# Kernel tuning notes

Measured on AMD Instinct MI355X. Metric: run time of the kernel, lower is better.

## Reference

```python
import jax, jax.numpy as jnp
import numpy as np

N_NODES = 100000
N_EDGES = 800000
IN_DIM = 128
HID = 128
EMB = 2 * HID  # 256, embedding_dim = hidden_dim * 2
N_CLS = 16


def _glorot(key, shape):
    fan_in, fan_out = shape
    lim = jnp.sqrt(6.0 / (fan_in + fan_out)).astype(jnp.float32)
    return jax.random.uniform(key, shape, jnp.float32, -lim, lim)


def setup_inputs() -> dict:
    key = jax.random.key(0)
    ks = jax.random.split(key, 12)
    x = jax.random.normal(ks[0], (N_NODES, IN_DIM), jnp.float32)
    edge_index = jax.random.randint(ks[1], (2, N_EDGES), 0, N_NODES, jnp.int64)
    return {
        "x": x,
        "edge_index": edge_index,
        # layer 1: GraphConv(IN_DIM -> HID)
        "W_rel1": _glorot(ks[2], (IN_DIM, HID)),
        "W_root1": _glorot(ks[3], (IN_DIM, HID)),
        "b1": jnp.zeros((HID,), jnp.float32),
        # layer 2: GraphConv(HID -> EMB)
        "W_rel2": _glorot(ks[4], (HID, EMB)),
        "W_root2": _glorot(ks[5], (HID, EMB)),
        "b2": jnp.zeros((EMB,), jnp.float32),
        # layer 3: GraphConv(EMB -> N_CLS)
        "W_rel3": _glorot(ks[6], (EMB, N_CLS)),
        "W_root3": _glorot(ks[7], (EMB, N_CLS)),
        "b3": jnp.zeros((N_CLS,), jnp.float32),
    }


def _graph_conv(x, src, dst, W_rel, W_root, b):
    # PyG GraphConv: out = lin_rel(sum_{j in N(i)} x_j) + lin_root(x_i)
    agg = jax.ops.segment_sum(x[src], dst, num_segments=N_NODES)  # [N, F_in]
    return agg @ W_rel + x @ W_root + b


def reference(x, edge_index, W_rel1, W_root1, b1, W_rel2, W_root2, b2,
              W_rel3, W_root3, b3):
    src, dst = edge_index[0], edge_index[1]
    h = jax.nn.relu(_graph_conv(x, src, dst, W_rel1, W_root1, b1))
    # dropout skipped: eval mode (training=False)
    h = jax.nn.relu(_graph_conv(h, src, dst, W_rel2, W_root2, b2))
    h = _graph_conv(h, src, dst, W_rel3, W_root3, b3)
    return jax.nn.log_softmax(h, axis=1)
```

## Files before the change

### kernel.cpp

```cpp
#include <hip/hip_runtime.h>

#define NN 100000
#define NE 800000
#define NPAD 100096
#define OCT 12544

typedef __attribute__((ext_vector_type(8))) __bf16 bf16x8;
typedef __attribute__((ext_vector_type(4))) float f32x4;

__device__ __forceinline__ uint f2bf(float f) {
  uint u = __float_as_uint(f);
  return (u + 0x7fffu + ((u >> 16) & 1u)) >> 16;
}
__device__ __forceinline__ float bflo(uint u) { return __uint_as_float(u << 16); }
__device__ __forceinline__ float bfhi(uint u) { return __uint_as_float(u & 0xffff0000u); }

__device__ __forceinline__ bf16x8 cvt8(float4 a, float4 b) {
  uint4 u;
  u.x = f2bf(a.x) | (f2bf(a.y) << 16);
  u.y = f2bf(a.z) | (f2bf(a.w) << 16);
  u.z = f2bf(b.x) | (f2bf(b.y) << 16);
  u.w = f2bf(b.z) | (f2bf(b.w) << 16);
  return *(bf16x8*)&u;
}


__device__ __forceinline__ bf16x8 ldfrag(const ushort* base, int row, int kb) {
  int off = (row << 8) + (kb ^ ((row & 15) << 4));
  return *(const bf16x8*)((const char*)base + off);
}

__global__ __launch_bounds__(512, 4) void k_fuse1(
    const float* __restrict__ x, ushort* __restrict__ Y1, ushort* __restrict__ Z1,
    const float* __restrict__ Wr1, const float* __restrict__ Wo1,
    const float* __restrict__ Wr2, const float* __restrict__ Wo2,
    const float* __restrict__ Wr3, const float* __restrict__ Wo3,
    ushort* __restrict__ wt, const int* __restrict__ dst, int* __restrict__ deg) {
  __shared__ ushort sW[128 * 128];
  int b = blockIdx.x;
  int tid = threadIdx.x;

  if (b >= 2352) {
    int idx = 32768 + (b - 2352) * 512 + tid;
    float v;
    if (idx < 98304) {
      const float* W;
      int base;
      if (idx < 65536) { W = Wr2; base = 32768; }
      else { W = Wo2; base = 65536; }
      int li = idx - base;
      int o = li >> 7, k = li & 127;
      k = (k & 7) * 16 + (k >> 3);
      v = W[(size_t)k * 256 + o];
    } else {
      int li = idx - 98304;
      int o = li >> 8, p = li & 255;
      int k = (p & 15) * 16 + (p >> 4);
      v = (o < 16) ? Wr3[(size_t)k * 16 + o] : Wo3[(size_t)k * 16 + (o - 16)];
    }
    wt[idx] = (ushort)f2bf(v);
    return;
  }
  if (b >= 784) {
    int hb = b - 784;
    int xcd = hb & 7, chunk = hb >> 3;
    int e0 = chunk * 4096 + tid;
#pragma unroll
    for (int i = 0; i < 8; ++i) {
      int e = e0 + i * 512;
      if (e < NE) {
        int d = dst[e];
        if (d / OCT == xcd) atomicAdd(&deg[d], 1);
      }
    }
    return;
  }

  int half = (b >> 3) & 1;
  int pr = (b >> 4) * 8 + (b & 7);
  if (pr >= NPAD / 256) return;
  int r0 = pr * 256;

  int lane = tid & 63, wid = tid >> 6;
  int cl = lane & 15, hi = lane >> 4;
  int arow0 = r0 + wid * 32 + cl;
  int arow1 = arow0 + 16;
  const float* px0 = x + (size_t)(arow0 < NN ? arow0 : NN - 1) * 128;
  const float* px1 = x + (size_t)(arow1 < NN ? arow1 : NN - 1) * 128;

  float4 F0[2][2], F1[2][2];
#pragma unroll
  for (int s = 0; s < 2; ++s) {
    F0[s][0] = *(const float4*)(px0 + s * 32 + hi * 8);
    F0[s][1] = *(const float4*)(px0 + s * 32 + hi * 8 + 4);
    F1[s][0] = *(const float4*)(px1 + s * 32 + hi * 8);
    F1[s][1] = *(const float4*)(px1 + s * 32 + hi * 8 + 4);
  }

  {
    const float* Wsrc = half ? Wo1 : Wr1;
    int o = tid & 127;
    int kp = tid >> 7;
#pragma unroll
    for (int it = 0; it < 16; ++it) {
      int k0 = (it * 4 + kp) * 2;
      float w0 = Wsrc[(size_t)k0 * 128 + o];
      float w1 = Wsrc[(size_t)(k0 + 1) * 128 + o];
      uint u = f2bf(w0) | (f2bf(w1) << 16);
      int byte = (o << 8) + ((((k0 >> 3) << 4) ^ ((o & 15) << 4))) + (k0 & 7) * 2;
      *(uint*)((char*)sW + byte) = u;
    }
  }
  __syncthreads();

  f32x4 zero = {0.f, 0.f, 0.f, 0.f};
  f32x4 acc0[8], acc1[8];
#pragma unroll
  for (int j = 0; j < 8; ++j) { acc0[j] = zero; acc1[j] = zero; }

#pragma unroll
  for (int ks = 0; ks < 4; ++ks) {
    const int p2 = ks & 1;
    bf16x8 A0 = cvt8(F0[p2][0], F0[p2][1]);
    bf16x8 A1 = cvt8(F1[p2][0], F1[p2][1]);
    int kb = ks * 64 + hi * 16;
#pragma unroll
    for (int j = 0; j < 8; ++j) {
      bf16x8 wf = ldfrag(sW, j * 16 + cl, kb);
      acc0[j] = __builtin_amdgcn_mfma_f32_16x16x32_bf16(A0, wf, acc0[j], 0, 0, 0);
      acc1[j] = __builtin_amdgcn_mfma_f32_16x16x32_bf16(A1, wf, acc1[j], 0, 0, 0);
    }
    if (ks < 2) {
      F0[p2][0] = *(const float4*)(px0 + (ks + 2) * 32 + hi * 8);
      F0[p2][1] = *(const float4*)(px0 + (ks + 2) * 32 + hi * 8 + 4);
      F1[p2][0] = *(const float4*)(px1 + (ks + 2) * 32 + hi * 8);
      F1[p2][1] = *(const float4*)(px1 + (ks + 2) * 32 + hi * 8 + 4);
    }
  }

  ushort* tgt = half ? Z1 : Y1;
#pragma unroll
  for (int i = 0; i < 2; ++i) {
#pragma unroll
    for (int reg = 0; reg < 4; ++reg) {
      int row = r0 + wid * 32 + i * 16 + hi * 4 + reg;
      if (row < NN) {
        float a[8];
#pragma unroll
        for (int j = 0; j < 8; ++j) a[j] = i ? acc1[j][reg] : acc0[j][reg];
        uint4 u;
        u.x = f2bf(a[0]) | (f2bf(a[1]) << 16);
        u.y = f2bf(a[2]) | (f2bf(a[3]) << 16);
        u.z = f2bf(a[4]) | (f2bf(a[5]) << 16);
        u.w = f2bf(a[6]) | (f2bf(a[7]) << 16);
        *(uint4*)(tgt + (size_t)row * 128 + cl * 8) = u;
      }
    }
  }
}

__global__ void k_scan_partial(const int* __restrict__ deg, int* __restrict__ bsum, int N) {
  __shared__ int s[256];
  int b = blockIdx.x, t = threadIdx.x;
  int base = b * 1024 + t * 4;
  int v = 0;
#pragma unroll
  for (int i = 0; i < 4; ++i) { int idx = base + i; if (idx < N) v += deg[idx]; }
  s[t] = v; __syncthreads();
  for (int o = 128; o > 0; o >>= 1) { if (t < o) s[t] += s[t + o]; __syncthreads(); }
  if (t == 0) bsum[b] = s[0];
}

__global__ void k_scan_final(const int* __restrict__ deg, const int* __restrict__ bsum,
                             int* __restrict__ offsets, int* __restrict__ cursor,
                             int N, int NB) {
  __shared__ int s2[128];
  __shared__ int s[256];
  int b = blockIdx.x, t = threadIdx.x;
  if (t < 128) s2[t] = (t < NB) ? bsum[t] : 0;
  __syncthreads();
  for (int o = 1; o < 128; o <<= 1) {
    int add = (t < 128 && t >= o) ? s2[t - o] : 0;
    __syncthreads();
    if (t < 128) s2[t] += add;
    __syncthreads();
  }
  int bpre = (b > 0) ? s2[b - 1] : 0;
  if (b == 0 && t == 0) offsets[N] = s2[NB - 1];

  int base = b * 1024 + t * 4;
  int v[4];
#pragma unroll
  for (int i = 0; i < 4; ++i) { int idx = base + i; v[i] = (idx < N) ? deg[idx] : 0; }
  int tsum = v[0] + v[1] + v[2] + v[3];
  s[t] = tsum; __syncthreads();
  for (int o = 1; o < 256; o <<= 1) {
    int add = (t >= o) ? s[t - o] : 0;
    __syncthreads();
    s[t] += add;
    __syncthreads();
  }
  int run = s[t] - tsum + bpre;
#pragma unroll
  for (int i = 0; i < 4; ++i) {
    int idx = base + i;
    if (idx < N) { offsets[idx] = run; cursor[idx] = run; }
    run += v[i];
  }
}

__global__ __launch_bounds__(256) void k_scatter(const int* __restrict__ src,
                                                 const int* __restrict__ dst,
                                                 int* __restrict__ cursor,
                                                 int* __restrict__ csr_src) {
  int xcd = blockIdx.x & 7, chunk = blockIdx.x >> 3;
  int e0 = chunk * 2048 + threadIdx.x;
#pragma unroll
  for (int i = 0; i < 8; ++i) {
    int e = e0 + i * 256;
    if (e < NE) {
      int d = dst[e];
      if (d / OCT == xcd) {
        int pos = atomicAdd(&cursor[d], 1);
        csr_src[pos] = src[e];
      }
    }
  }
}

#define ACC8(q)                      \
  do {                               \
    acc[0] += bflo(q.x); acc[1] += bfhi(q.x); \
    acc[2] += bflo(q.y); acc[3] += bfhi(q.y); \
    acc[4] += bflo(q.z); acc[5] += bfhi(q.z); \
    acc[6] += bflo(q.w); acc[7] += bfhi(q.w); \
  } while (0)

#define GATHER8(X4)                                               \
  int j = o0;                                                     \
  if (j + 7 < o1) {                                               \
    uint4 q0 = X4[(size_t)csr[j] * 16 + fl];                      \
    uint4 q1 = X4[(size_t)csr[j + 1] * 16 + fl];                  \
    uint4 q2 = X4[(size_t)csr[j + 2] * 16 + fl];                  \
    uint4 q3 = X4[(size_t)csr[j + 3] * 16 + fl];                  \
    uint4 q4 = X4[(size_t)csr[j + 4] * 16 + fl];                  \
    uint4 q5 = X4[(size_t)csr[j + 5] * 16 + fl];                  \
    uint4 q6 = X4[(size_t)csr[j + 6] * 16 + fl];                  \
    uint4 q7 = X4[(size_t)csr[j + 7] * 16 + fl];                  \
    j += 8;                                                       \
    while (j + 7 < o1) {                                          \
      uint4 p0 = X4[(size_t)csr[j] * 16 + fl];                    \
      uint4 p1 = X4[(size_t)csr[j + 1] * 16 + fl];                \
      uint4 p2 = X4[(size_t)csr[j + 2] * 16 + fl];                \
      uint4 p3 = X4[(size_t)csr[j + 3] * 16 + fl];                \
      uint4 p4 = X4[(size_t)csr[j + 4] * 16 + fl];                \
      uint4 p5 = X4[(size_t)csr[j + 5] * 16 + fl];                \
      uint4 p6 = X4[(size_t)csr[j + 6] * 16 + fl];                \
      uint4 p7 = X4[(size_t)csr[j + 7] * 16 + fl];                \
      j += 8;                                                     \
      ACC8(q0); ACC8(q1); ACC8(q2); ACC8(q3);                     \
      ACC8(q4); ACC8(q5); ACC8(q6); ACC8(q7);                     \
      q0 = p0; q1 = p1; q2 = p2; q3 = p3;                         \
      q4 = p4; q5 = p5; q6 = p6; q7 = p7;                         \
    }                                                             \
    ACC8(q0); ACC8(q1); ACC8(q2); ACC8(q3);                       \
    ACC8(q4); ACC8(q5); ACC8(q6); ACC8(q7);                       \
  }                                                               \
  if (j + 3 < o1) {                                               \
    uint4 q0 = X4[(size_t)csr[j] * 16 + fl];                      \
    uint4 q1 = X4[(size_t)csr[j + 1] * 16 + fl];                  \
    uint4 q2 = X4[(size_t)csr[j + 2] * 16 + fl];                  \
    uint4 q3 = X4[(size_t)csr[j + 3] * 16 + fl];                  \
    j += 4;                                                       \
    ACC8(q0); ACC8(q1); ACC8(q2); ACC8(q3);                       \
  }                                                               \
  for (; j < o1; ++j) {                                           \
    uint4 q = X4[(size_t)csr[j] * 16 + fl];                       \
    ACC8(q);                                                      \
  }

__global__ __launch_bounds__(256) void k_agg_relu(const ushort* __restrict__ Y1,
                                                  const ushort* __restrict__ Z1,
                                                  const int* __restrict__ offsets,
                                                  const int* __restrict__ csr,
                                                  const float* __restrict__ bias,
                                                  ushort* __restrict__ h1) {
  int tid = threadIdx.x;
  int sg = tid >> 4, fl = tid & 15;
  int n = blockIdx.x * 16 + sg;
  if (n >= NN) return;
  int o0 = offsets[n], o1 = offsets[n + 1];
  const uint4* X4 = (const uint4*)Y1;
  float acc[8];
#pragma unroll
  for (int k = 0; k < 8; ++k) acc[k] = 0.f;
  GATHER8(X4)
  uint4 zown = ((const uint4*)Z1)[(size_t)n * 16 + fl];
  float z[8] = {bflo(zown.x), bfhi(zown.x), bflo(zown.y), bfhi(zown.y),
                bflo(zown.z), bfhi(zown.z), bflo(zown.w), bfhi(zown.w)};
  float r[8];
#pragma unroll
  for (int jj = 0; jj < 8; ++jj) {
    r[jj] = fmaxf(acc[jj] + z[jj] + bias[jj * 16 + fl], 0.f);
  }
  uint4 o;
  o.x = f2bf(r[0]) | (f2bf(r[1]) << 16);
  o.y = f2bf(r[2]) | (f2bf(r[3]) << 16);
  o.z = f2bf(r[4]) | (f2bf(r[5]) << 16);
  o.w = f2bf(r[6]) | (f2bf(r[7]) << 16);
  ((uint4*)h1)[(size_t)n * 16 + fl] = o;
}

__global__ __launch_bounds__(256) void k_aggbf(const ushort* __restrict__ X,
                                               const int* __restrict__ offsets,
                                               const int* __restrict__ csr,
                                               ushort* __restrict__ out) {
  int tid = threadIdx.x;
  int sg = tid >> 4, fl = tid & 15;
  int n = blockIdx.x * 16 + sg;
  if (n >= NN) return;
  int o0 = offsets[n], o1 = offsets[n + 1];
  const uint4* X4 = (const uint4*)X;
  float acc[8];
#pragma unroll
  for (int k = 0; k < 8; ++k) acc[k] = 0.f;
  GATHER8(X4)
  uint4 o;
  o.x = f2bf(acc[0]) | (f2bf(acc[1]) << 16);
  o.y = f2bf(acc[2]) | (f2bf(acc[3]) << 16);
  o.z = f2bf(acc[4]) | (f2bf(acc[5]) << 16);
  o.w = f2bf(acc[6]) | (f2bf(acc[7]) << 16);
  ((uint4*)out)[(size_t)n * 16 + fl] = o;
}

__global__ __launch_bounds__(512, 4) void k_gemm2l3(
    const ushort* __restrict__ Aagg, const ushort* __restrict__ Aroot,
    const ushort* __restrict__ Wrelt, const ushort* __restrict__ Wroott,
    const float* __restrict__ bias2, const ushort* __restrict__ Wt3,
    const float* __restrict__ bias3, ushort* __restrict__ y3b, float* __restrict__ z) {
  __shared__ ushort sW[256 * 128];
  int tid = threadIdx.x;
  int r0 = blockIdx.x * 128;
  int lane = tid & 63, wid = tid >> 6;
  int cl = lane & 15, hi = lane >> 4;
  int arow = r0 + wid * 16 + cl;
  const ushort* pa = Aagg + (size_t)arow * 128 + hi * 8;
  const ushort* pr = Aroot + (size_t)arow * 128 + hi * 8;

  bf16x8 Aa[2], Ar[2];
  Aa[0] = *(const bf16x8*)(pa);
  Aa[1] = *(const bf16x8*)(pa + 32);
  Ar[0] = *(const bf16x8*)(pr);
  Ar[1] = *(const bf16x8*)(pr + 32);

  {
    const char* gw = (const char*)Wrelt;
#pragma unroll
    for (int i = 0; i < 8; ++i) {
      int L = (tid + i * 512) << 4;
      int row = L >> 8;
      int gb = L ^ ((row & 15) << 4);
      __builtin_amdgcn_global_load_lds((const __attribute__((address_space(1))) void*)(gw + gb),
                                       (__attribute__((address_space(3))) void*)((char*)sW + L), 16, 0, 0);
    }
  }
  __syncthreads();

  f32x4 zero = {0.f, 0.f, 0.f, 0.f};
  f32x4 acc[16];
#pragma unroll
  for (int j = 0; j < 16; ++j) acc[j] = zero;

#pragma unroll
  for (int ks = 0; ks < 4; ++ks) {
    const int p = ks & 1;
    int kb = ks * 64 + hi * 16;
#pragma unroll
    for (int j = 0; j < 16; ++j) {
      bf16x8 wf = ldfrag(sW, j * 16 + cl, kb);
      acc[j] = __builtin_amdgcn_mfma_f32_16x16x32_bf16(Aa[p], wf, acc[j], 0, 0, 0);
    }
    if (ks < 2) Aa[p] = *(const bf16x8*)(pa + (ks + 2) * 32);
  }
  __syncthreads();

  {
    const char* gw = (const char*)Wroott;
#pragma unroll
    for (int i = 0; i < 8; ++i) {
      int L = (tid + i * 512) << 4;
      int row = L >> 8;
      int gb = L ^ ((row & 15) << 4);
      __builtin_amdgcn_global_load_lds((const __attribute__((address_space(1))) void*)(gw + gb),
                                       (__attribute__((address_space(3))) void*)((char*)sW + L), 16, 0, 0);
    }
  }
  __syncthreads();

#pragma unroll
  for (int ks = 0; ks < 4; ++ks) {
    const int p = ks & 1;
    int kb = ks * 64 + hi * 16;
#pragma unroll
    for (int j = 0; j < 16; ++j) {
      bf16x8 wf = ldfrag(sW, j * 16 + cl, kb);
      acc[j] = __builtin_amdgcn_mfma_f32_16x16x32_bf16(Ar[p], wf, acc[j], 0, 0, 0);
    }
    if (ks < 2) Ar[p] = *(const bf16x8*)(pr + (ks + 2) * 32);
  }
  __syncthreads();

  {
    float bv[16];
#pragma unroll
    for (int j = 0; j < 16; ++j) bv[j] = bias2[j * 16 + cl];
#pragma unroll
    for (int reg = 0; reg < 4; ++reg) {
      int rr = hi * 4 + reg;
      float v[16];
#pragma unroll
      for (int j = 0; j < 16; ++j) v[j] = fmaxf(acc[j][reg] + bv[j], 0.f);
      uint4 a, bq;
      a.x = f2bf(v[0]) | (f2bf(v[1]) << 16);
      a.y = f2bf(v[2]) | (f2bf(v[3]) << 16);
      a.z = f2bf(v[4]) | (f2bf(v[5]) << 16);
      a.w = f2bf(v[6]) | (f2bf(v[7]) << 16);
      bq.x = f2bf(v[8]) | (f2bf(v[9]) << 16);
      bq.y = f2bf(v[10]) | (f2bf(v[11]) << 16);
      bq.z = f2bf(v[12]) | (f2bf(v[13]) << 16);
      bq.w = f2bf(v[14]) | (f2bf(v[15]) << 16);
      int rowb = (wid * 16 + rr) * 512;
      *(uint4*)((char*)sW + rowb + ((cl * 32 + 0) ^ (rr << 4))) = a;
      *(uint4*)((char*)sW + rowb + ((cl * 32 + 16) ^ (rr << 4))) = bq;
    }
  }
  __syncthreads();

  f32x4 ay = zero, az = zero;
  const ushort* w3a = Wt3 + cl * 256 + hi * 8;
  const ushort* w3b = Wt3 + (16 + cl) * 256 + hi * 8;
#pragma unroll
  for (int ks = 0; ks < 8; ++ks) {
    int c = ks * 4 + hi;
    bf16x8 a = *(const bf16x8*)((const char*)sW + (wid * 16 + cl) * 512 + ((c * 16) ^ (cl << 4)));
    bf16x8 b0 = *(const bf16x8*)(w3a + ks * 32);
    bf16x8 b1 = *(const bf16x8*)(w3b + ks * 32);
    ay = __builtin_amdgcn_mfma_f32_16x16x32_bf16(a, b0, ay, 0, 0, 0);
    az = __builtin_amdgcn_mfma_f32_16x16x32_bf16(a, b1, az, 0, 0, 0);
  }
  float bv3 = bias3[cl];
#pragma unroll
  for (int reg = 0; reg < 4; ++reg) {
    int row = r0 + wid * 16 + hi * 4 + reg;
    if (row < NN) {
      y3b[(size_t)row * 16 + cl] = (ushort)f2bf(ay[reg]);
      z[(size_t)row * 16 + cl] = az[reg] + bv3;
    }
  }
}

__global__ void k_agg16lsm(const int* __restrict__ offsets, const int* __restrict__ csr,
                           const ushort* __restrict__ y3b, float* __restrict__ out) {
  int t = blockIdx.x * 256 + threadIdx.x;
  if (t >= NN * 8) return;
  int n = t >> 3, g = t & 7;
  int o0 = offsets[n], o1 = offsets[n + 1];
  float a0 = 0.f, a1 = 0.f;
  const uint* Y = (const uint*)y3b;
  int j = o0;
  if (j + 3 < o1) {
    uint u0 = Y[(size_t)csr[j] * 8 + g];
    uint u1 = Y[(size_t)csr[j + 1] * 8 + g];
    uint u2 = Y[(size_t)csr[j + 2] * 8 + g];
    uint u3 = Y[(size_t)csr[j + 3] * 8 + g];
    j += 4;
    while (j + 3 < o1) {
      uint v0 = Y[(size_t)csr[j] * 8 + g];
      uint v1 = Y[(size_t)csr[j + 1] * 8 + g];
      uint v2 = Y[(size_t)csr[j + 2] * 8 + g];
      uint v3 = Y[(size_t)csr[j + 3] * 8 + g];
      j += 4;
      a0 += bflo(u0) + bflo(u1) + bflo(u2) + bflo(u3);
      a1 += bfhi(u0) + bfhi(u1) + bfhi(u2) + bfhi(u3);
      u0 = v0; u1 = v1; u2 = v2; u3 = v3;
    }
    a0 += bflo(u0) + bflo(u1) + bflo(u2) + bflo(u3);
    a1 += bfhi(u0) + bfhi(u1) + bfhi(u2) + bfhi(u3);
  }
  for (; j < o1; ++j) {
    uint u = Y[(size_t)csr[j] * 8 + g];
    a0 += bflo(u); a1 += bfhi(u);
  }
  float v0 = out[n * 16 + g * 2] + a0;
  float v1 = out[n * 16 + g * 2 + 1] + a1;
  float m = fmaxf(v0, v1);
#pragma unroll
  for (int mask = 1; mask < 8; mask <<= 1) m = fmaxf(m, __shfl_xor(m, mask));
  float s = __expf(v0 - m) + __expf(v1 - m);
#pragma unroll
  for (int mask = 1; mask < 8; mask <<= 1) s += __shfl_xor(s, mask);
  float ls = __logf(s);
  out[n * 16 + g * 2] = v0 - m - ls;
  out[n * 16 + g * 2 + 1] = v1 - m - ls;
}

extern "C" void kernel_launch(void* const* d_in, const int* in_sizes, int n_in,
                              void* d_out, int out_size, void* d_ws, size_t ws_size,
                              hipStream_t stream) {
  const float* x = (const float*)d_in[0];
  const int* ei = (const int*)d_in[1];
  const float* Wrel1 = (const float*)d_in[2];
  const float* Wroot1 = (const float*)d_in[3];
  const float* b1 = (const float*)d_in[4];
  const float* Wrel2 = (const float*)d_in[5];
  const float* Wroot2 = (const float*)d_in[6];
  const float* b2 = (const float*)d_in[7];
  const float* Wrel3 = (const float*)d_in[8];
  const float* Wroot3 = (const float*)d_in[9];
  const float* b3 = (const float*)d_in[10];
  float* out = (float*)d_out;

  char* ws = (char*)d_ws;
  size_t off = 0;
  auto alloc = [&](size_t bytes) {
    void* p = ws + off;
    off += (bytes + 255) / 256 * 256;
    return p;
  };
  int* deg = (int*)alloc((size_t)NN * 4);
  int* offsets = (int*)alloc((size_t)(NN + 1) * 4);
  int* cursor = (int*)alloc((size_t)NN * 4);
  int* bsum = (int*)alloc(128 * 4);
  int* csr = (int*)alloc((size_t)NE * 4);
  ushort* Y1 = (ushort*)alloc((size_t)NN * 128 * 2);
  ushort* Z1 = (ushort*)alloc((size_t)NN * 128 * 2);
  ushort* aggb = (ushort*)alloc((size_t)NPAD * 128 * 2);
  ushort* h1b = (ushort*)alloc((size_t)NPAD * 128 * 2);
  ushort* y3b = (ushort*)alloc((size_t)NN * 16 * 2);
  ushort* wt = (ushort*)alloc((size_t)106496 * 2);
  ushort *Wr2t = wt + 32768, *Wo2t = wt + 65536;
  ushort* Wt3 = wt + 98304;

  const int* src = ei;
  const int* dst = ei + NE;

  hipMemsetAsync(deg, 0, (size_t)NN * 4, stream);
  k_fuse1<<<2496, 512, 0, stream>>>(x, Y1, Z1, Wrel1, Wroot1, Wrel2, Wroot2, Wrel3,
                                    Wroot3, wt, dst, deg);

  int NB = (NN + 1023) / 1024;
  k_scan_partial<<<NB, 256, 0, stream>>>(deg, bsum, NN);
  k_scan_final<<<NB, 256, 0, stream>>>(deg, bsum, offsets, cursor, NN, NB);
  int nchunk = (NE + 2047) / 2048;
  k_scatter<<<8 * nchunk, 256, 0, stream>>>(src, dst, cursor, csr);

  k_agg_relu<<<NN / 16, 256, 0, stream>>>(Y1, Z1, offsets, csr, b1, h1b);
  k_aggbf<<<(NN + 15) / 16, 256, 0, stream>>>(h1b, offsets, csr, aggb);
  k_gemm2l3<<<NPAD / 128, 512, 0, stream>>>(aggb, h1b, Wr2t, Wo2t, b2, Wt3, b3, y3b, out);
  k_agg16lsm<<<(NN * 8 + 255) / 256, 256, 0, stream>>>(offsets, csr, y3b, out);
}
```

Before: 224.0 us.

## Sort nodes into degree bins so aggregation warps process similar-degree nodes

Builds a degree histogram during the scan, prefix-sums it, and scatters node ids into a degree-binned permutation. The three aggregation kernels then visit nodes in that permuted order, so nodes sharing a wavefront have similar neighbor counts. This is meant to reduce divergence and load imbalance inside wavefronts. It adds two small kernels plus atomics, gives up locality of node-ordered output writes and Z1 reads, and the binning atomics make the order nondeterministic.

```diff
diff --git a/kernel.cpp b/kernel.cpp
--- a/kernel.cpp
+++ b/kernel.cpp
@@ -159,9 +159,11 @@
   }
 }
 
-__global__ void k_scan_partial(const int* __restrict__ deg, int* __restrict__ bsum, int N) {
+__global__ void k_scan_partial(const int* __restrict__ deg, int* __restrict__ bsum,
+                               int* __restrict__ dbins, int N) {
   __shared__ int s[256];
   int b = blockIdx.x, t = threadIdx.x;
+  if (b == 0 && t < 64) dbins[t] = 0;
   int base = b * 1024 + t * 4;
   int v = 0;
 #pragma unroll
@@ -173,11 +175,13 @@
 
 __global__ void k_scan_final(const int* __restrict__ deg, const int* __restrict__ bsum,
                              int* __restrict__ offsets, int* __restrict__ cursor,
-                             int N, int NB) {
+                             int* __restrict__ dbins, int N, int NB) {
   __shared__ int s2[128];
   __shared__ int s[256];
+  __shared__ int hist[64];
   int b = blockIdx.x, t = threadIdx.x;
   if (t < 128) s2[t] = (t < NB) ? bsum[t] : 0;
+  if (t < 64) hist[t] = 0;
   __syncthreads();
   for (int o = 1; o < 128; o <<= 1) {
     int add = (t < 128 && t >= o) ? s2[t - o] : 0;
@@ -191,7 +195,11 @@
   int base = b * 1024 + t * 4;
   int v[4];
 #pragma unroll
-  for (int i = 0; i < 4; ++i) { int idx = base + i; v[i] = (idx < N) ? deg[idx] : 0; }
+  for (int i = 0; i < 4; ++i) {
+    int idx = base + i;
+    v[i] = (idx < N) ? deg[idx] : 0;
+    if (idx < N) atomicAdd(&hist[v[i] < 63 ? v[i] : 63], 1);
+  }
   int tsum = v[0] + v[1] + v[2] + v[3];
   s[t] = tsum; __syncthreads();
   for (int o = 1; o < 256; o <<= 1) {
@@ -206,6 +214,36 @@
     int idx = base + i;
     if (idx < N) { offsets[idx] = run; cursor[idx] = run; }
     run += v[i];
+  }
+  if (t < 64 && hist[t]) atomicAdd(&dbins[t], hist[t]);
+}
+
+__global__ void k_dscan(const int* __restrict__ dbins, int* __restrict__ dcur) {
+  __shared__ int s[64];
+  int t = threadIdx.x;
+  int v = dbins[t];
+  s[t] = v; __syncthreads();
+  for (int o = 1; o < 64; o <<= 1) {
+    int add = (t >= o) ? s[t - o] : 0;
+    __syncthreads();
+    s[t] += add;
+    __syncthreads();
+  }
+  dcur[t] = s[t] - v;
+}
+
+__global__ void k_dscatter(const int* __restrict__ offsets, int* __restrict__ dcur,
+                           int* __restrict__ perm, int N) {
+  int base = blockIdx.x * 1024 + threadIdx.x * 4;
+#pragma unroll
+  for (int i = 0; i < 4; ++i) {
+    int idx = base + i;
+    if (idx < N) {
+      int d = offsets[idx + 1] - offsets[idx];
+      int bin = d < 63 ? d : 63;
+      int pos = atomicAdd(&dcur[bin], 1);
+      perm[pos] = idx;
+    }
   }
 }
 
@@ -283,12 +321,14 @@
                                                   const ushort* __restrict__ Z1,
                                                   const int* __restrict__ offsets,
                                                   const int* __restrict__ csr,
+                                                  const int* __restrict__ perm,
                                                   const float* __restrict__ bias,
                                                   ushort* __restrict__ h1) {
   int tid = threadIdx.x;
   int sg = tid >> 4, fl = tid & 15;
-  int n = blockIdx.x * 16 + sg;
-  if (n >= NN) return;
+  int idx = blockIdx.x * 16 + sg;
+  if (idx >= NN) return;
+  int n = perm[idx];
   int o0 = offsets[n], o1 = offsets[n + 1];
   const uint4* X4 = (const uint4*)Y1;
   float acc[8];
@@ -314,11 +354,13 @@
 __global__ __launch_bounds__(256) void k_aggbf(const ushort* __restrict__ X,
                                                const int* __restrict__ offsets,
                                                const int* __restrict__ csr,
+                                               const int* __restrict__ perm,
                                                ushort* __restrict__ out) {
   int tid = threadIdx.x;
   int sg = tid >> 4, fl = tid & 15;
-  int n = blockIdx.x * 16 + sg;
-  if (n >= NN) return;
+  int idx = blockIdx.x * 16 + sg;
+  if (idx >= NN) return;
+  int n = perm[idx];
   int o0 = offsets[n], o1 = offsets[n + 1];
   const uint4* X4 = (const uint4*)X;
   float acc[8];
@@ -460,10 +502,12 @@
 }
 
 __global__ void k_agg16lsm(const int* __restrict__ offsets, const int* __restrict__ csr,
+                           const int* __restrict__ perm,
                            const ushort* __restrict__ y3b, float* __restrict__ out) {
   int t = blockIdx.x * 256 + threadIdx.x;
   if (t >= NN * 8) return;
-  int n = t >> 3, g = t & 7;
+  int n = perm[t >> 3];
+  int g = t & 7;
   int o0 = offsets[n], o1 = offsets[n + 1];
   float a0 = 0.f, a1 = 0.f;
   const uint* Y = (const uint*)y3b;
@@ -531,6 +575,9 @@
   int* offsets = (int*)alloc((size_t)(NN + 1) * 4);
   int* cursor = (int*)alloc((size_t)NN * 4);
   int* bsum = (int*)alloc(128 * 4);
+  int* dbins = (int*)alloc(64 * 4);
+  int* dcur = (int*)alloc(64 * 4);
+  int* perm = (int*)alloc((size_t)NN * 4);
   int* csr = (int*)alloc((size_t)NE * 4);
   ushort* Y1 = (ushort*)alloc((size_t)NN * 128 * 2);
   ushort* Z1 = (ushort*)alloc((size_t)NN * 128 * 2);
@@ -549,13 +596,15 @@
                                     Wroot3, wt, dst, deg);
 
   int NB = (NN + 1023) / 1024;
-  k_scan_partial<<<NB, 256, 0, stream>>>(deg, bsum, NN);
-  k_scan_final<<<NB, 256, 0, stream>>>(deg, bsum, offsets, cursor, NN, NB);
+  k_scan_partial<<<NB, 256, 0, stream>>>(deg, bsum, dbins, NN);
+  k_scan_final<<<NB, 256, 0, stream>>>(deg, bsum, offsets, cursor, dbins, NN, NB);
   int nchunk = (NE + 2047) / 2048;
   k_scatter<<<8 * nchunk, 256, 0, stream>>>(src, dst, cursor, csr);
-
-  k_agg_relu<<<NN / 16, 256, 0, stream>>>(Y1, Z1, offsets, csr, b1, h1b);
-  k_aggbf<<<(NN + 15) / 16, 256, 0, stream>>>(h1b, offsets, csr, aggb);
+  k_dscan<<<1, 64, 0, stream>>>(dbins, dcur);
+  k_dscatter<<<NB, 256, 0, stream>>>(offsets, dcur, perm, NN);
+
+  k_agg_relu<<<NN / 16, 256, 0, stream>>>(Y1, Z1, offsets, csr, perm, b1, h1b);
+  k_aggbf<<<(NN + 15) / 16, 256, 0, stream>>>(h1b, offsets, csr, perm, aggb);
   k_gemm2l3<<<NPAD / 128, 512, 0, stream>>>(aggb, h1b, Wr2t, Wo2t, b2, Wt3, b3, y3b, out);
-  k_agg16lsm<<<(NN * 8 + 255) / 256, 256, 0, stream>>>(offsets, csr, y3b, out);
-}
+  k_agg16lsm<<<(NN * 8 + 255) / 256, 256, 0, stream>>>(offsets, csr, perm, y3b, out);
+}
```

Measured after the change: 579.0 us. +158.5%, slower.
